# Performance work log

Hardware: AMD Instinct MI355X
Metric: run time of the kernel (lower is better)

The kernel has to match this reference:

```python
import jax, jax.numpy as jnp
import numpy as np

B, S, E = 2, 2048, 1024
H, D = 16, 64
BASE = 10000.0


def rotate_half(x):
    x1, x2 = jnp.split(x, 2, axis=-1)
    return jnp.concatenate((-x2, x1), axis=-1)


def rope_cos_sin(seq_len, dim):
    inv_freq = 1.0 / (BASE ** (jnp.arange(0, dim, 2, dtype=jnp.float32) / dim))
    t = jnp.arange(seq_len, dtype=jnp.float32)
    freqs = jnp.einsum('i,j->ij', t, inv_freq)          # [S, D/2]
    emb = jnp.concatenate((freqs, freqs), axis=-1)       # [S, D]
    return jnp.cos(emb), jnp.sin(emb)


def setup_inputs() -> dict:
    key = jax.random.key(0)
    ks = jax.random.split(key, 9)
    s = 1.0 / np.sqrt(E)
    inp = {
        'x': jax.random.normal(ks[0], (B, S, E), dtype=jnp.float32),
        'mask': jnp.ones((B, S), dtype=jnp.int32),
        'Wq': jax.random.normal(ks[1], (E, H * D), dtype=jnp.float32) * s,
        'bq': jnp.zeros((H * D,), dtype=jnp.float32),
        'Wk': jax.random.normal(ks[2], (E, H * D), dtype=jnp.float32) * s,
        'bk': jnp.zeros((H * D,), dtype=jnp.float32),
        'Wv': jax.random.normal(ks[3], (E, H * D), dtype=jnp.float32) * s,
        'bv': jnp.zeros((H * D,), dtype=jnp.float32),
        'Wo': jax.random.normal(ks[4], (H * D, E), dtype=jnp.float32) * s,
        'bo': jnp.zeros((E,), dtype=jnp.float32),
    }
    return inp


def reference(x, mask, Wq, bq, Wk, bk, Wv, bv, Wo, bo):
    b, s, _ = x.shape
    scale = D ** (-0.5)
    # projections -> [B, H, S, D]
    q = (x @ Wq + bq).reshape(b, s, H, D).transpose(0, 2, 1, 3)
    k = (x @ Wk + bk).reshape(b, s, H, D).transpose(0, 2, 1, 3)
    v = (x @ Wv + bv).reshape(b, s, H, D).transpose(0, 2, 1, 3)
    # rotary position embedding
    cos, sin = rope_cos_sin(s, D)                      # [S, D]
    cos = cos[None, None]
    sin = sin[None, None]
    q = q * cos + rotate_half(q) * sin
    k = k * cos + rotate_half(k) * sin
    # scores [B, H, S, S]
    scores = jnp.einsum('bhqd,bhkd->bhqk', q, k) * scale
    # padding mask [B,1,1,S]
    scores = jnp.where(mask[:, None, None, :] == 0, -jnp.inf, scores)
    # causal mask
    i = jnp.arange(s)
    causal = jnp.where(i[None, :] > i[:, None], -jnp.inf, 0.0)  # [S, S]
    scores = scores + causal[None, None]
    attn = jax.nn.softmax(scores, axis=-1)
    ctx = jnp.einsum('bhqk,bhkd->bhqd', attn, v)
    ctx = ctx.transpose(0, 2, 1, 3).reshape(b, s, H * D)
    return ctx @ Wo + bo
```

## Files before the change

kernel.cpp:

```cpp
#include <hip/hip_runtime.h>
#include <cstdint>
#include <cstddef>

#define DEVI __device__ __forceinline__

typedef __bf16 bf16_t;
typedef __bf16 bf16x4 __attribute__((ext_vector_type(4)));
typedef __bf16 bf16x8 __attribute__((ext_vector_type(8)));
typedef float  f32x4  __attribute__((ext_vector_type(4)));
typedef float  f32x16 __attribute__((ext_vector_type(16)));
typedef unsigned short u16x4 __attribute__((ext_vector_type(4)));
typedef unsigned int   u32x4 __attribute__((ext_vector_type(4)));

static constexpr int Bz = 2, S = 2048, E = 1024, H = 16, Dh = 64;
static constexpr int M  = Bz * S;
static constexpr int N  = H * Dh;
static constexpr int Kd = E;

DEVI unsigned short f2bf(float f) {
  unsigned u = __builtin_bit_cast(unsigned, f);
  return (unsigned short)((u + 0x7fffu + ((u >> 16) & 1u)) >> 16);
}

DEVI void async_copy16(void* lds, const void* g) {
  __builtin_amdgcn_global_load_lds((__attribute__((address_space(1))) void*)(g),
                                   (__attribute__((address_space(3))) void*)(lds), 16, 0, 0);
}

DEVI void block_sync() { asm volatile("s_barrier" ::: "memory"); }
#define VMCNT4() asm volatile("s_waitcnt vmcnt(4)" ::: "memory")
#define VMCNT0() asm volatile("s_waitcnt vmcnt(0)" ::: "memory")

DEVI unsigned cvtpk(float lo, float hi) {
  unsigned r;
  asm("v_cvt_pk_bf16_f32 %0, %1, %2" : "=v"(r) : "v"(lo), "v"(hi));
  return r;
}
DEVI void swap32(unsigned& x, unsigned& y) {
  asm("v_permlane32_swap_b32 %0, %1" : "+v"(x), "+v"(y));
}

__global__ void prep_kernel(const float* __restrict__ x, bf16_t* __restrict__ xb,
                            const float* __restrict__ Wq, const float* __restrict__ Wk,
                            const float* __restrict__ Wv, const float* __restrict__ Wo,
                            bf16_t* __restrict__ WtBase,
                            float* __restrict__ ropeC, float* __restrict__ ropeS) {
  __shared__ unsigned short tile[64][68];
  const int blk = blockIdx.x, tid = threadIdx.x;
  if (blk < 4096) {
    int i = blk * 256 + tid;
    float4 v = ((const float4*)x)[i];
    u16x4 o = { f2bf(v.x), f2bf(v.y), f2bf(v.z), f2bf(v.w) };
    ((u16x4*)xb)[i] = o;
  } else if (blk < 5120) {
    const int i = blk - 4096;
    const int z = i >> 8, rest = i & 255;
    const int n0 = (rest & 15) * 64, k0 = (rest >> 4) * 64;
    const float* W = (z == 0) ? Wq : (z == 1) ? Wk : (z == 2) ? Wv : Wo;
    unsigned short* T = (unsigned short*)(WtBase + (size_t)z * Kd * N);
    for (int e = tid; e < 1024; e += 256) {
      int r = e >> 4, c4 = (e & 15) * 4;
      float4 v = *(const float4*)(W + (size_t)(k0 + r) * N + n0 + c4);
      u16x4 o = { f2bf(v.x), f2bf(v.y), f2bf(v.z), f2bf(v.w) };
      *(u16x4*)&tile[r][c4] = o;
    }
    __syncthreads();
    for (int e = tid; e < 1024; e += 256) {
      int r = e >> 4, c4 = (e & 15) * 4;
      u16x4 o = { tile[c4][r], tile[c4 + 1][r], tile[c4 + 2][r], tile[c4 + 3][r] };
      *(u16x4*)&T[(size_t)(n0 + r) * Kd + k0 + c4] = o;
    }
  } else {
    int i = (blk - 5120) * 256 + tid;
    int pos = i >> 5, j = i & 31;
    float inv = exp2f(-(float)j * 0.41524101186092029f);
    float ang = (float)pos * inv;
    ropeC[i] = cosf(ang);
    ropeS[i] = sinf(ang);
  }
}

__global__ void vtrans_kernel(const bf16_t* __restrict__ V, bf16_t* __restrict__ Vt) {
  __shared__ unsigned short tile[64][68];
  const int bh = blockIdx.y;
  const int s0 = blockIdx.x * 64;
  const unsigned short* Vp = (const unsigned short*)V + (size_t)bh * S * Dh;
  unsigned short* Tp = (unsigned short*)Vt + (size_t)bh * Dh * S;
  const int tid = threadIdx.x;
  for (int e = tid; e < 1024; e += 256) {
    int r = e >> 4, c4 = (e & 15) * 4;
    u16x4 v = *(const u16x4*)(Vp + (size_t)(s0 + r) * Dh + c4);
    *(u16x4*)&tile[r][c4] = v;
  }
  __syncthreads();
  for (int e = tid; e < 1024; e += 256) {
    int d = e >> 4, s4 = (e & 15) * 4;
    u16x4 o = { tile[s4][d], tile[s4 + 1][d], tile[s4 + 2][d], tile[s4 + 3][d] };
    *(u16x4*)&Tp[(size_t)d * S + s0 + s4] = o;
  }
}


DEVI void gemm_mainloop(const bf16_t* __restrict__ A, const bf16_t* __restrict__ Bt,
                        bf16_t* sA, bf16_t* sB, int m0, int n0, f32x4 (&acc)[4][4]) {
  const int tid  = threadIdx.x;
  const int lane = tid & 63;
  const int wid  = tid >> 6;
  const int l16  = lane & 15;
  const int quad = lane >> 4;
  const int wm = (wid >> 1) * 64;
  const int wn = (wid & 1) * 64;
  const int o0 = wid * 2048 + lane * 16;
  const int o1 = o0 + 1024;
  const int r0 = o0 >> 6, c0 = o0 & 63;
  const int r1 = o1 >> 6, c1 = o1 & 63;
  const char* Ab = (const char*)A;
  const char* Bb = (const char*)Bt;
  char* sAc = (char*)sA;
  char* sBc = (char*)sB;

  for (int k0 = 0; k0 < Kd; k0 += 32) {
    __syncthreads();
    async_copy16(sAc + wid * 2048,        Ab + ((size_t)(m0 + r0) * Kd + k0) * 2 + c0);
    async_copy16(sAc + wid * 2048 + 1024, Ab + ((size_t)(m0 + r1) * Kd + k0) * 2 + c1);
    async_copy16(sBc + wid * 2048,        Bb + ((size_t)(n0 + r0) * Kd + k0) * 2 + c0);
    async_copy16(sBc + wid * 2048 + 1024, Bb + ((size_t)(n0 + r1) * Kd + k0) * 2 + c1);
    __syncthreads();
    bf16x8 af[4], bfv[4];
#pragma unroll
    for (int mi = 0; mi < 4; ++mi)
      af[mi] = *(const bf16x8*)(sA + (wm + mi * 16 + l16) * 32 + quad * 8);
#pragma unroll
    for (int ni = 0; ni < 4; ++ni)
      bfv[ni] = *(const bf16x8*)(sB + (wn + ni * 16 + l16) * 32 + quad * 8);
#pragma unroll
    for (int mi = 0; mi < 4; ++mi)
#pragma unroll
      for (int ni = 0; ni < 4; ++ni)
        acc[mi][ni] = __builtin_amdgcn_mfma_f32_16x16x32_bf16(af[mi], bfv[ni], acc[mi][ni], 0, 0, 0);
  }
}

__global__ __launch_bounds__(256, 3) void gemm_qkv_kernel(
    const bf16_t* __restrict__ xb, const bf16_t* __restrict__ WtBase,
    const float* __restrict__ bq, const float* __restrict__ bk, const float* __restrict__ bv,
    bf16_t* __restrict__ outBase,
    const float* __restrict__ ropeC, const float* __restrict__ ropeS) {
  __shared__ bf16_t sA[4096], sB[4096];
  const int z = blockIdx.z;
  const bf16_t* Bt = WtBase + (size_t)z * Kd * N;
  const float* bias = (z == 0) ? bq : (z == 1) ? bk : bv;
  unsigned short* outp = (unsigned short*)(outBase + (size_t)z * M * N);
  const int n0 = blockIdx.x * 128, m0 = blockIdx.y * 128;
  f32x4 acc[4][4] = {};
  gemm_mainloop(xb, Bt, sA, sB, m0, n0, acc);

  const int tid = threadIdx.x, lane = tid & 63, wid = tid >> 6;
  const int l16 = lane & 15, quad = lane >> 4;
  const int wm = (wid >> 1) * 64, wn = (wid & 1) * 64;
  const int cbase = n0 + wn;
  const int h = cbase >> 6;

  if (z < 2) {
    const float qs = (z == 0) ? 0.18033688011112042f : 1.0f;
#pragma unroll
    for (int mi = 0; mi < 4; ++mi)
#pragma unroll
      for (int r = 0; r < 4; ++r) {
        int t = m0 + wm + mi * 16 + quad * 4 + r;
        int bb = t >> 11, s = t & (S - 1);
        size_t obase = ((size_t)(bb * H + h) * S + s) * Dh;
#pragma unroll
        for (int np = 0; np < 2; ++np) {
          int j = np * 16 + l16;
          float cc = ropeC[s * 32 + j];
          float ss = ropeS[s * 32 + j];
          float xlo = acc[mi][np][r]     + bias[cbase + j];
          float xhi = acc[mi][np + 2][r] + bias[cbase + j + 32];
          outp[obase + j]      = f2bf((xlo * cc - xhi * ss) * qs);
          outp[obase + j + 32] = f2bf((xhi * cc + xlo * ss) * qs);
        }
      }
  } else {
#pragma unroll
    for (int mi = 0; mi < 4; ++mi)
#pragma unroll
      for (int r = 0; r < 4; ++r) {
        int t = m0 + wm + mi * 16 + quad * 4 + r;
        int bb = t >> 11, s = t & (S - 1);
        size_t obase = ((size_t)(bb * H + h) * S + s) * Dh;
#pragma unroll
        for (int ni = 0; ni < 4; ++ni) {
          int d = ni * 16 + l16;
          outp[obase + d] = f2bf(acc[mi][ni][r] + bias[cbase + d]);
        }
      }
  }
}

__global__ __launch_bounds__(256, 4) void gemm_o_kernel(
    const bf16_t* __restrict__ A, const bf16_t* __restrict__ Bt,
    const float* __restrict__ bias, float* __restrict__ out) {
  __shared__ bf16_t sA[2048], sB[4096];
  const int n0 = blockIdx.x * 128, m0 = blockIdx.y * 64;
  const int tid = threadIdx.x, lane = tid & 63, wid = tid >> 6;
  const int l16 = lane & 15, quad = lane >> 4;
  const int wm = (wid >> 1) * 32, wn = (wid & 1) * 64;
  const int rowoff = lane >> 2, col8 = (lane & 3) * 8;
  const char* Ab = (const char*)A;
  const char* Bb = (const char*)Bt;
  char* sAc = (char*)sA;
  char* sBc = (char*)sB;
  f32x4 acc[2][4] = {};

  for (int k0 = 0; k0 < Kd; k0 += 32) {
    __syncthreads();
    async_copy16(sAc + wid * 1024,
                 Ab + ((size_t)(m0 + wid * 16 + rowoff) * Kd + k0 + col8) * 2);
    async_copy16(sBc + (wid * 2) * 1024,
                 Bb + ((size_t)(n0 + wid * 32 + rowoff) * Kd + k0 + col8) * 2);
    async_copy16(sBc + (wid * 2 + 1) * 1024,
                 Bb + ((size_t)(n0 + wid * 32 + 16 + rowoff) * Kd + k0 + col8) * 2);
    __syncthreads();
    bf16x8 af[2], bfv[4];
#pragma unroll
    for (int mi = 0; mi < 2; ++mi)
      af[mi] = *(const bf16x8*)(sA + (wm + mi * 16 + l16) * 32 + quad * 8);
#pragma unroll
    for (int ni = 0; ni < 4; ++ni)
      bfv[ni] = *(const bf16x8*)(sB + (wn + ni * 16 + l16) * 32 + quad * 8);
#pragma unroll
    for (int mi = 0; mi < 2; ++mi)
#pragma unroll
      for (int ni = 0; ni < 4; ++ni)
        acc[mi][ni] = __builtin_amdgcn_mfma_f32_16x16x32_bf16(af[mi], bfv[ni], acc[mi][ni], 0, 0, 0);
  }
#pragma unroll
  for (int mi = 0; mi < 2; ++mi)
#pragma unroll
    for (int r = 0; r < 4; ++r) {
      int t = m0 + wm + mi * 16 + quad * 4 + r;
#pragma unroll
      for (int ni = 0; ni < 4; ++ni) {
        int c = n0 + wn + ni * 16 + l16;
        out[(size_t)t * N + c] = acc[mi][ni][r] + bias[c];
      }
    }
}

template <bool MASKED>
DEVI void attn32_phase(const bf16_t* __restrict__ Qp, const char* __restrict__ Kg,
                       const char* __restrict__ Vg, const int* __restrict__ mp,
                       unsigned short* __restrict__ cp, char* lds,
                       int b, int bh, int qb) {
  const int tid = threadIdx.x, lane = tid & 63, wid = tid >> 6;
  const int grp = wid >> 2, w4 = wid & 3;
  const int l32 = lane & 31, hi = lane >> 5;

  const int qw = qb * 128 + w4 * 32;
  const int qg = qw + l32;
  const int nTot = 2 * (qb + 1);
  const int qd = nTot >> 2, rm = nTot & 3;
  const int nG  = qd + ((grp < rm) ? 1 : 0);
  const int st0 = grp * qd + ((grp < rm) ? grp : rm);
  const int nMax = qd + (rm ? 1 : 0);
  const int gk0 = st0 * 64;
  char* gB = lds + grp * 32768;

  bf16x8 qf[4];
#pragma unroll
  for (int c = 0; c < 4; ++c)
    qf[c] = *(const bf16x8*)(Qp + (size_t)(qw + l32) * Dh + c * 16 + hi * 8);
  asm volatile("" :: "v"((float)qf[3][7]));

  int kLds[2], vLds[2], kOff[2], vOff[2];
#pragma unroll
  for (int i = 0; i < 2; ++i) {
    const int s = w4 * 2 + i;
    const int a = s >> 2, c = s & 3;
    kLds[i] = s * 1024;
    kOff[i] = ((a * 32 + l32) * Dh + c * 16 + hi * 8) * 2;
    vLds[i] = 8192 + s * 1024;
    vOff[i] = ((s >> 2) * 32 + l32) * (S * 2) + (((s & 3) * 16 + hi * 8) * 2);
  }

  f32x16 cacc0 = {}, cacc1 = {};
  float lsum = 0.f;

  if (nG > 0) {
    const char* ks = Kg + (size_t)gk0 * (Dh * 2);
    const char* vs = Vg + (size_t)gk0 * 2;
    async_copy16(gB + kLds[0], ks + kOff[0]);
    async_copy16(gB + kLds[1], ks + kOff[1]);
    async_copy16(gB + vLds[0], vs + vOff[0]);
    async_copy16(gB + vLds[1], vs + vOff[1]);
  }

  for (int kt = 0; kt < nMax; ++kt) {
    const int cur = kt & 1;
    const int kb = gk0 + kt * 64;
    const bool act = kt < nG;
    unsigned long long dm = 0;
    if (act) {
      if (kt + 1 < nG) {
        char* dst = gB + (cur ^ 1) * 16384;
        const char* ks = Kg + (size_t)(kb + 64) * (Dh * 2);
        const char* vs = Vg + (size_t)(kb + 64) * 2;
        async_copy16(dst + kLds[0], ks + kOff[0]);
        async_copy16(dst + kLds[1], ks + kOff[1]);
        async_copy16(dst + vLds[0], vs + vOff[0]);
        async_copy16(dst + vLds[1], vs + vOff[1]);
        if (!MASKED) { VMCNT4(); }
      } else if (!MASKED) {
        VMCNT0();
      }
      if (MASKED) {
        int mk = mp[kb + lane];
        VMCNT0();
        dm = __ballot(mk == 0);
      }
    }
    block_sync();

    if (act) {
      const bf16_t* sK = (const bf16_t*)(gB + cur * 16384);
      const bf16_t* sV = (const bf16_t*)(gB + cur * 16384 + 8192);
      const bool needC = (kb + 63 > qw);

#pragma unroll
      for (int a = 0; a < 2; ++a) {
        f32x16 st = {};
        __builtin_amdgcn_s_setprio(1);
#pragma unroll
        for (int c = 0; c < 4; ++c) {
          bf16x8 kf = *(const bf16x8*)(sK + (a * 4 + c) * 512 + lane * 8);
          st = __builtin_amdgcn_mfma_f32_32x32x16_bf16(kf, qf[c], st, 0, 0, 0);
        }
        __builtin_amdgcn_s_setprio(0);
        if (MASKED && dm) {
#pragma unroll
          for (int r = 0; r < 16; ++r)
            if ((dm >> (a * 32 + (r & 3) + 8 * (r >> 2) + 4 * hi)) & 1ull) st[r] = -1e30f;
        }
        if (needC) {
          const int kbase = kb + a * 32 + 4 * hi - qg;
#pragma unroll
          for (int r = 0; r < 16; ++r)
            if (kbase + (r & 3) + 8 * (r >> 2) > 0) st[r] = -1e30f;
        }
        unsigned P0[4], P1[4];
#pragma unroll
        for (int m = 0; m < 4; ++m) {
          float p0 = exp2f(st[4 * m + 0]), p1 = exp2f(st[4 * m + 1]);
          float p2 = exp2f(st[4 * m + 2]), p3 = exp2f(st[4 * m + 3]);
          lsum += (p0 + p1) + (p2 + p3);
          P0[m] = cvtpk(p0, p1);
          P1[m] = cvtpk(p2, p3);
        }
        swap32(P0[0], P0[1]); swap32(P1[0], P1[1]);
        swap32(P0[2], P0[3]); swap32(P1[2], P1[3]);
        u32x4 t0 = { P0[0], P1[0], P0[1], P1[1] };
        u32x4 t1 = { P0[2], P1[2], P0[3], P1[3] };
        const bf16x8 f0 = __builtin_bit_cast(bf16x8, t0);
        const bf16x8 f1 = __builtin_bit_cast(bf16x8, t1);
        __builtin_amdgcn_s_setprio(1);
        {
          bf16x8 v00 = *(const bf16x8*)(sV + (0 + a * 2 + 0) * 512 + lane * 8);
          cacc0 = __builtin_amdgcn_mfma_f32_32x32x16_bf16(v00, f0, cacc0, 0, 0, 0);
          bf16x8 v01 = *(const bf16x8*)(sV + (0 + a * 2 + 1) * 512 + lane * 8);
          cacc0 = __builtin_amdgcn_mfma_f32_32x32x16_bf16(v01, f1, cacc0, 0, 0, 0);
          bf16x8 v10 = *(const bf16x8*)(sV + (4 + a * 2 + 0) * 512 + lane * 8);
          cacc1 = __builtin_amdgcn_mfma_f32_32x32x16_bf16(v10, f0, cacc1, 0, 0, 0);
          bf16x8 v11 = *(const bf16x8*)(sV + (4 + a * 2 + 1) * 512 + lane * 8);
          cacc1 = __builtin_amdgcn_mfma_f32_32x32x16_bf16(v11, f1, cacc1, 0, 0, 0);
        }
        __builtin_amdgcn_s_setprio(0);
      }
    }
    block_sync();
  }

  if (grp != 0) {
    char* rb = lds + (size_t)((grp - 1) * 4 + w4) * 8448;
#pragma unroll
    for (int c = 0; c < 4; ++c) {
      f32x4 v = { cacc0[4 * c], cacc0[4 * c + 1], cacc0[4 * c + 2], cacc0[4 * c + 3] };
      *(f32x4*)(rb + c * 1024 + lane * 16) = v;
    }
#pragma unroll
    for (int c = 0; c < 4; ++c) {
      f32x4 v = { cacc1[4 * c], cacc1[4 * c + 1], cacc1[4 * c + 2], cacc1[4 * c + 3] };
      *(f32x4*)(rb + (4 + c) * 1024 + lane * 16) = v;
    }
    *(float*)(rb + 8192 + lane * 4) = lsum;
  }
  asm volatile("s_waitcnt lgkmcnt(0)" ::: "memory");
  block_sync();
  if (grp == 0) {
#pragma unroll
    for (int j = 1; j < 4; ++j) {
      const char* rb = lds + (size_t)((j - 1) * 4 + w4) * 8448;
#pragma unroll
      for (int c = 0; c < 4; ++c) {
        f32x4 v = *(const f32x4*)(rb + c * 1024 + lane * 16);
        cacc0[4 * c] += v[0]; cacc0[4 * c + 1] += v[1];
        cacc0[4 * c + 2] += v[2]; cacc0[4 * c + 3] += v[3];
      }
#pragma unroll
      for (int c = 0; c < 4; ++c) {
        f32x4 v = *(const f32x4*)(rb + (4 + c) * 1024 + lane * 16);
        cacc1[4 * c] += v[0]; cacc1[4 * c + 1] += v[1];
        cacc1[4 * c + 2] += v[2]; cacc1[4 * c + 3] += v[3];
      }
      lsum += *(const float*)(rb + 8192 + lane * 4);
    }
    lsum += __shfl_xor(lsum, 32);
    const float inv = 1.0f / lsum;
    const size_t base = ((size_t)(b * S + qw + l32)) * N + (size_t)(bh & 15) * Dh;
#pragma unroll
    for (int m = 0; m < 4; ++m) {
      const int d0 = m * 8 + 4 * hi;
      u16x4 o0 = { f2bf(cacc0[4 * m + 0] * inv), f2bf(cacc0[4 * m + 1] * inv),
                   f2bf(cacc0[4 * m + 2] * inv), f2bf(cacc0[4 * m + 3] * inv) };
      *(u16x4*)&cp[base + d0] = o0;
      u16x4 o1 = { f2bf(cacc1[4 * m + 0] * inv), f2bf(cacc1[4 * m + 1] * inv),
                   f2bf(cacc1[4 * m + 2] * inv), f2bf(cacc1[4 * m + 3] * inv) };
      *(u16x4*)&cp[base + 32 + d0] = o1;
    }
  }
  block_sync();
}

__global__ __launch_bounds__(1024, 4) void attn_kernel(
    const bf16_t* __restrict__ Q, const bf16_t* __restrict__ Kb,
    const bf16_t* __restrict__ Vt, const int* __restrict__ mask,
    bf16_t* __restrict__ ctx) {
  __shared__ f32x4 ldsbuf[8192];

  const int idx = blockIdx.x;
  const int p   = idx >> 5;
  const int bh  = idx & 31;
  const int qbL = 15 - p, qbS = p;
  const int b   = bh >> 4;
  const int lane = threadIdx.x & 63;

  const bf16_t* Qp = Q + (size_t)bh * S * Dh;
  const char*   Kg = (const char*)(Kb + (size_t)bh * S * Dh);
  const char*   Vg = (const char*)(Vt + (size_t)bh * Dh * S);
  const int*    mp = mask + b * S;

  int dead = 0;
  const int4* mp4 = (const int4*)mp;
  for (int c = lane; c < S / 4; c += 64) {
    int4 m = mp4[c];
    dead |= (m.x == 0) | (m.y == 0) | (m.z == 0) | (m.w == 0);
  }
  const bool anydead = __ballot(dead != 0) != 0ull;

  unsigned short* cp = (unsigned short*)ctx;
  char* lds = (char*)ldsbuf;
  if (!anydead) {
#pragma unroll 1
    for (int t = 0; t < 2; ++t)
      attn32_phase<false>(Qp, Kg, Vg, mp, cp, lds, b, bh, t ? qbS : qbL);
  } else {
#pragma unroll 1
    for (int t = 0; t < 2; ++t)
      attn32_phase<true>(Qp, Kg, Vg, mp, cp, lds, b, bh, t ? qbS : qbL);
  }
}


extern "C" void kernel_launch(void* const* d_in, const int* in_sizes, int n_in,
                              void* d_out, int out_size, void* d_ws, size_t ws_size,
                              hipStream_t stream) {
  const float* x  = (const float*)d_in[0];
  const int*  msk = (const int*)d_in[1];
  const float* Wq = (const float*)d_in[2];
  const float* bq = (const float*)d_in[3];
  const float* Wk = (const float*)d_in[4];
  const float* bk = (const float*)d_in[5];
  const float* Wv = (const float*)d_in[6];
  const float* bv = (const float*)d_in[7];
  const float* Wo = (const float*)d_in[8];
  const float* bo = (const float*)d_in[9];
  float* out = (float*)d_out;
  (void)in_sizes; (void)n_in; (void)out_size; (void)ws_size;

  char* ws = (char*)d_ws;
  bf16_t* xb   = (bf16_t*)(ws);
  bf16_t* WT   = (bf16_t*)(ws + (8u  << 20));
  bf16_t* qkv  = (bf16_t*)(ws + (16u << 20));
  bf16_t* Qb   = qkv;
  bf16_t* Kbuf = qkv + (size_t)1 * M * N;
  bf16_t* Vb   = qkv + (size_t)2 * M * N;
  bf16_t* Vt   = xb;
  bf16_t* ctx  = Vb;
  float* ropeC = (float*)(ws + (40u << 20));
  float* ropeS = ropeC + (size_t)S * 32;

  prep_kernel<<<5376, 256, 0, stream>>>(x, xb, Wq, Wk, Wv, Wo, WT, ropeC, ropeS);
  gemm_qkv_kernel<<<dim3(8, 32, 3), 256, 0, stream>>>(xb, WT, bq, bk, bv, qkv, ropeC, ropeS);
  vtrans_kernel<<<dim3(32, 32), 256, 0, stream>>>(Vb, Vt);
  attn_kernel<<<256, 1024, 0, stream>>>(Qb, Kbuf, Vt, msk, ctx);
  gemm_o_kernel<<<dim3(8, 64), 256, 0, stream>>>(ctx, WT + (size_t)3 * Kd * N, bo, out);
}
```

Measured before the change: 224.2 us.

## Split attention into 64-query tiles with 512-thread blocks and swizzled LDS reduction

Attention now runs 512 blocks of 512 threads. Each block handles 64-query tiles instead of 128-query tiles, with four key-split groups of two waves, and each group steps through 32-key chunks. One wave of each pair loads K and the other loads V. The cross-group reduction now lands in a swizzled LDS layout, and all waves share the final sum and bf16 store instead of only group 0. This is meant to raise the block count and spread the causal work more evenly across CUs, with a cheaper reduction, at the cost of more barriers per key chunk and smaller MFMA batches per sync.

```diff
diff --git a/kernel.cpp b/kernel.cpp
--- a/kernel.cpp
+++ b/kernel.cpp
@@ -252,20 +252,20 @@
 DEVI void attn32_phase(const bf16_t* __restrict__ Qp, const char* __restrict__ Kg,
                        const char* __restrict__ Vg, const int* __restrict__ mp,
                        unsigned short* __restrict__ cp, char* lds,
-                       int b, int bh, int qb) {
+                       int b, int bh, int qt) {
   const int tid = threadIdx.x, lane = tid & 63, wid = tid >> 6;
-  const int grp = wid >> 2, w4 = wid & 3;
+  const int grp = wid >> 1, w2 = wid & 1;
   const int l32 = lane & 31, hi = lane >> 5;
 
-  const int qw = qb * 128 + w4 * 32;
+  const int qw = qt * 64 + w2 * 32;
   const int qg = qw + l32;
-  const int nTot = 2 * (qb + 1);
-  const int qd = nTot >> 2, rm = nTot & 3;
+  const int nk = 2 * (qt + 1);
+  const int qd = nk >> 2, rm = nk & 3;
   const int nG  = qd + ((grp < rm) ? 1 : 0);
   const int st0 = grp * qd + ((grp < rm) ? grp : rm);
   const int nMax = qd + (rm ? 1 : 0);
-  const int gk0 = st0 * 64;
-  char* gB = lds + grp * 32768;
+  const int gk0 = st0 * 32;
+  char* gB = lds + grp * 16384;
 
   bf16x8 qf[4];
 #pragma unroll
@@ -273,49 +273,45 @@
     qf[c] = *(const bf16x8*)(Qp + (size_t)(qw + l32) * Dh + c * 16 + hi * 8);
   asm volatile("" :: "v"((float)qf[3][7]));
 
-  int kLds[2], vLds[2], kOff[2], vOff[2];
-#pragma unroll
-  for (int i = 0; i < 2; ++i) {
-    const int s = w4 * 2 + i;
-    const int a = s >> 2, c = s & 3;
-    kLds[i] = s * 1024;
-    kOff[i] = ((a * 32 + l32) * Dh + c * 16 + hi * 8) * 2;
-    vLds[i] = 8192 + s * 1024;
-    vOff[i] = ((s >> 2) * 32 + l32) * (S * 2) + (((s & 3) * 16 + hi * 8) * 2);
+  const char* gsrc = w2 ? Vg : Kg;
+  const size_t keyB = w2 ? 2u : 128u;
+  int sLds[4], sOff[4];
+#pragma unroll
+  for (int i = 0; i < 4; ++i) {
+    sLds[i] = (w2 * 4 + i) * 1024;
+    if (w2 == 0) sOff[i] = (l32 * 64 + i * 16 + hi * 8) * 2;
+    else {
+      int e = i >> 1, kc = i & 1;
+      sOff[i] = ((e * 32 + l32) * S + kc * 16 + hi * 8) * 2;
+    }
   }
 
   f32x16 cacc0 = {}, cacc1 = {};
   float lsum = 0.f;
 
   if (nG > 0) {
-    const char* ks = Kg + (size_t)gk0 * (Dh * 2);
-    const char* vs = Vg + (size_t)gk0 * 2;
-    async_copy16(gB + kLds[0], ks + kOff[0]);
-    async_copy16(gB + kLds[1], ks + kOff[1]);
-    async_copy16(gB + vLds[0], vs + vOff[0]);
-    async_copy16(gB + vLds[1], vs + vOff[1]);
+    const char* bp = gsrc + (size_t)gk0 * keyB;
+#pragma unroll
+    for (int i = 0; i < 4; ++i) async_copy16(gB + sLds[i], bp + sOff[i]);
   }
 
   for (int kt = 0; kt < nMax; ++kt) {
     const int cur = kt & 1;
-    const int kb = gk0 + kt * 64;
+    const int kb = gk0 + kt * 32;
     const bool act = kt < nG;
     unsigned long long dm = 0;
     if (act) {
       if (kt + 1 < nG) {
-        char* dst = gB + (cur ^ 1) * 16384;
-        const char* ks = Kg + (size_t)(kb + 64) * (Dh * 2);
-        const char* vs = Vg + (size_t)(kb + 64) * 2;
-        async_copy16(dst + kLds[0], ks + kOff[0]);
-        async_copy16(dst + kLds[1], ks + kOff[1]);
-        async_copy16(dst + vLds[0], vs + vOff[0]);
-        async_copy16(dst + vLds[1], vs + vOff[1]);
+        const char* bp = gsrc + (size_t)(kb + 32) * keyB;
+        char* dst = gB + (cur ^ 1) * 8192;
+#pragma unroll
+        for (int i = 0; i < 4; ++i) async_copy16(dst + sLds[i], bp + sOff[i]);
         if (!MASKED) { VMCNT4(); }
       } else if (!MASKED) {
         VMCNT0();
       }
       if (MASKED) {
-        int mk = mp[kb + lane];
+        int mk = mp[kb + l32];
         VMCNT0();
         dm = __ballot(mk == 0);
       }
@@ -323,124 +319,108 @@
     block_sync();
 
     if (act) {
-      const bf16_t* sK = (const bf16_t*)(gB + cur * 16384);
-      const bf16_t* sV = (const bf16_t*)(gB + cur * 16384 + 8192);
-      const bool needC = (kb + 63 > qw);
-
-#pragma unroll
-      for (int a = 0; a < 2; ++a) {
-        f32x16 st = {};
-        __builtin_amdgcn_s_setprio(1);
-#pragma unroll
-        for (int c = 0; c < 4; ++c) {
-          bf16x8 kf = *(const bf16x8*)(sK + (a * 4 + c) * 512 + lane * 8);
-          st = __builtin_amdgcn_mfma_f32_32x32x16_bf16(kf, qf[c], st, 0, 0, 0);
-        }
-        __builtin_amdgcn_s_setprio(0);
-        if (MASKED && dm) {
-#pragma unroll
-          for (int r = 0; r < 16; ++r)
-            if ((dm >> (a * 32 + (r & 3) + 8 * (r >> 2) + 4 * hi)) & 1ull) st[r] = -1e30f;
-        }
-        if (needC) {
-          const int kbase = kb + a * 32 + 4 * hi - qg;
-#pragma unroll
-          for (int r = 0; r < 16; ++r)
-            if (kbase + (r & 3) + 8 * (r >> 2) > 0) st[r] = -1e30f;
-        }
-        unsigned P0[4], P1[4];
-#pragma unroll
-        for (int m = 0; m < 4; ++m) {
-          float p0 = exp2f(st[4 * m + 0]), p1 = exp2f(st[4 * m + 1]);
-          float p2 = exp2f(st[4 * m + 2]), p3 = exp2f(st[4 * m + 3]);
-          lsum += (p0 + p1) + (p2 + p3);
-          P0[m] = cvtpk(p0, p1);
-          P1[m] = cvtpk(p2, p3);
-        }
-        swap32(P0[0], P0[1]); swap32(P1[0], P1[1]);
-        swap32(P0[2], P0[3]); swap32(P1[2], P1[3]);
-        u32x4 t0 = { P0[0], P1[0], P0[1], P1[1] };
-        u32x4 t1 = { P0[2], P1[2], P0[3], P1[3] };
-        const bf16x8 f0 = __builtin_bit_cast(bf16x8, t0);
-        const bf16x8 f1 = __builtin_bit_cast(bf16x8, t1);
-        __builtin_amdgcn_s_setprio(1);
-        {
-          bf16x8 v00 = *(const bf16x8*)(sV + (0 + a * 2 + 0) * 512 + lane * 8);
-          cacc0 = __builtin_amdgcn_mfma_f32_32x32x16_bf16(v00, f0, cacc0, 0, 0, 0);
-          bf16x8 v01 = *(const bf16x8*)(sV + (0 + a * 2 + 1) * 512 + lane * 8);
-          cacc0 = __builtin_amdgcn_mfma_f32_32x32x16_bf16(v01, f1, cacc0, 0, 0, 0);
-          bf16x8 v10 = *(const bf16x8*)(sV + (4 + a * 2 + 0) * 512 + lane * 8);
-          cacc1 = __builtin_amdgcn_mfma_f32_32x32x16_bf16(v10, f0, cacc1, 0, 0, 0);
-          bf16x8 v11 = *(const bf16x8*)(sV + (4 + a * 2 + 1) * 512 + lane * 8);
-          cacc1 = __builtin_amdgcn_mfma_f32_32x32x16_bf16(v11, f1, cacc1, 0, 0, 0);
-        }
-        __builtin_amdgcn_s_setprio(0);
-      }
+      const bf16_t* sT = (const bf16_t*)(gB + cur * 8192);
+      f32x16 st = {};
+      __builtin_amdgcn_s_setprio(1);
+#pragma unroll
+      for (int c = 0; c < 4; ++c) {
+        bf16x8 kf = *(const bf16x8*)(sT + c * 512 + lane * 8);
+        st = __builtin_amdgcn_mfma_f32_32x32x16_bf16(kf, qf[c], st, 0, 0, 0);
+      }
+      __builtin_amdgcn_s_setprio(0);
+      if (MASKED && dm) {
+#pragma unroll
+        for (int r = 0; r < 16; ++r)
+          if ((dm >> ((r & 3) + 8 * (r >> 2) + 4 * hi)) & 1ull) st[r] = -1e30f;
+      }
+      if (kb + 31 > qw) {
+        const int kbase = kb + 4 * hi - qg;
+#pragma unroll
+        for (int r = 0; r < 16; ++r)
+          if (kbase + (r & 3) + 8 * (r >> 2) > 0) st[r] = -1e30f;
+      }
+      unsigned P0[4], P1[4];
+#pragma unroll
+      for (int m = 0; m < 4; ++m) {
+        float p0 = exp2f(st[4 * m + 0]), p1 = exp2f(st[4 * m + 1]);
+        float p2 = exp2f(st[4 * m + 2]), p3 = exp2f(st[4 * m + 3]);
+        lsum += (p0 + p1) + (p2 + p3);
+        P0[m] = cvtpk(p0, p1);
+        P1[m] = cvtpk(p2, p3);
+      }
+      swap32(P0[0], P0[1]); swap32(P1[0], P1[1]);
+      swap32(P0[2], P0[3]); swap32(P1[2], P1[3]);
+      u32x4 t0 = { P0[0], P1[0], P0[1], P1[1] };
+      u32x4 t1 = { P0[2], P1[2], P0[3], P1[3] };
+      const bf16x8 f0 = __builtin_bit_cast(bf16x8, t0);
+      const bf16x8 f1 = __builtin_bit_cast(bf16x8, t1);
+      __builtin_amdgcn_s_setprio(1);
+      {
+        bf16x8 v00 = *(const bf16x8*)(sT + 2048 + 0 * 512 + lane * 8);
+        cacc0 = __builtin_amdgcn_mfma_f32_32x32x16_bf16(v00, f0, cacc0, 0, 0, 0);
+        bf16x8 v01 = *(const bf16x8*)(sT + 2048 + 1 * 512 + lane * 8);
+        cacc0 = __builtin_amdgcn_mfma_f32_32x32x16_bf16(v01, f1, cacc0, 0, 0, 0);
+        bf16x8 v10 = *(const bf16x8*)(sT + 2048 + 2 * 512 + lane * 8);
+        cacc1 = __builtin_amdgcn_mfma_f32_32x32x16_bf16(v10, f0, cacc1, 0, 0, 0);
+        bf16x8 v11 = *(const bf16x8*)(sT + 2048 + 3 * 512 + lane * 8);
+        cacc1 = __builtin_amdgcn_mfma_f32_32x32x16_bf16(v11, f1, cacc1, 0, 0, 0);
+      }
+      __builtin_amdgcn_s_setprio(0);
     }
     block_sync();
   }
 
-  if (grp != 0) {
-    char* rb = lds + (size_t)((grp - 1) * 4 + w4) * 8448;
-#pragma unroll
-    for (int c = 0; c < 4; ++c) {
-      f32x4 v = { cacc0[4 * c], cacc0[4 * c + 1], cacc0[4 * c + 2], cacc0[4 * c + 3] };
-      *(f32x4*)(rb + c * 1024 + lane * 16) = v;
-    }
-#pragma unroll
-    for (int c = 0; c < 4; ++c) {
-      f32x4 v = { cacc1[4 * c], cacc1[4 * c + 1], cacc1[4 * c + 2], cacc1[4 * c + 3] };
-      *(f32x4*)(rb + (4 + c) * 1024 + lane * 16) = v;
-    }
-    *(float*)(rb + 8192 + lane * 4) = lsum;
+  float* reg = (float*)lds;
+  {
+    const int row = w2 * 32 + l32;
+    float* rb = reg + grp * 4096 + row * 64;
+#pragma unroll
+    for (int m = 0; m < 4; ++m) {
+      f32x4 v = { cacc0[4 * m], cacc0[4 * m + 1], cacc0[4 * m + 2], cacc0[4 * m + 3] };
+      *(f32x4*)(rb + ((8 * m + 4 * hi + 4 * row) & 63)) = v;
+    }
+#pragma unroll
+    for (int m = 0; m < 4; ++m) {
+      f32x4 v = { cacc1[4 * m], cacc1[4 * m + 1], cacc1[4 * m + 2], cacc1[4 * m + 3] };
+      *(f32x4*)(rb + ((32 + 8 * m + 4 * hi + 4 * row) & 63)) = v;
+    }
+    reg[16384 + (grp * 2 + hi) * 64 + row] = lsum;
   }
   asm volatile("s_waitcnt lgkmcnt(0)" ::: "memory");
   block_sync();
-  if (grp == 0) {
-#pragma unroll
-    for (int j = 1; j < 4; ++j) {
-      const char* rb = lds + (size_t)((j - 1) * 4 + w4) * 8448;
-#pragma unroll
-      for (int c = 0; c < 4; ++c) {
-        f32x4 v = *(const f32x4*)(rb + c * 1024 + lane * 16);
-        cacc0[4 * c] += v[0]; cacc0[4 * c + 1] += v[1];
-        cacc0[4 * c + 2] += v[2]; cacc0[4 * c + 3] += v[3];
-      }
-#pragma unroll
-      for (int c = 0; c < 4; ++c) {
-        f32x4 v = *(const f32x4*)(rb + (4 + c) * 1024 + lane * 16);
-        cacc1[4 * c] += v[0]; cacc1[4 * c + 1] += v[1];
-        cacc1[4 * c + 2] += v[2]; cacc1[4 * c + 3] += v[3];
-      }
-      lsum += *(const float*)(rb + 8192 + lane * 4);
-    }
-    lsum += __shfl_xor(lsum, 32);
-    const float inv = 1.0f / lsum;
-    const size_t base = ((size_t)(b * S + qw + l32)) * N + (size_t)(bh & 15) * Dh;
-#pragma unroll
-    for (int m = 0; m < 4; ++m) {
-      const int d0 = m * 8 + 4 * hi;
-      u16x4 o0 = { f2bf(cacc0[4 * m + 0] * inv), f2bf(cacc0[4 * m + 1] * inv),
-                   f2bf(cacc0[4 * m + 2] * inv), f2bf(cacc0[4 * m + 3] * inv) };
-      *(u16x4*)&cp[base + d0] = o0;
-      u16x4 o1 = { f2bf(cacc1[4 * m + 0] * inv), f2bf(cacc1[4 * m + 1] * inv),
-                   f2bf(cacc1[4 * m + 2] * inv), f2bf(cacc1[4 * m + 3] * inv) };
-      *(u16x4*)&cp[base + 32 + d0] = o1;
-    }
+  {
+    const int orow = wid * 8 + (lane & 7);
+    const int d0 = (lane >> 3) * 8;
+    f32x4 oa = {}, ob = {};
+    float ls = 0.f;
+#pragma unroll
+    for (int g = 0; g < 4; ++g) {
+      const float* rb = reg + g * 4096 + orow * 64;
+      f32x4 va = *(const f32x4*)(rb + ((d0 + 4 * orow) & 63));
+      f32x4 vb = *(const f32x4*)(rb + ((d0 + 4 + 4 * orow) & 63));
+      oa += va; ob += vb;
+      ls += reg[16384 + (g * 2 + 0) * 64 + orow] + reg[16384 + (g * 2 + 1) * 64 + orow];
+    }
+    const float inv = 1.0f / ls;
+    const size_t base = ((size_t)(b * S + qt * 64 + orow)) * N + (size_t)(bh & 15) * Dh + d0;
+    u16x4 o0 = { f2bf(oa[0] * inv), f2bf(oa[1] * inv), f2bf(oa[2] * inv), f2bf(oa[3] * inv) };
+    u16x4 o1 = { f2bf(ob[0] * inv), f2bf(ob[1] * inv), f2bf(ob[2] * inv), f2bf(ob[3] * inv) };
+    *(u16x4*)&cp[base] = o0;
+    *(u16x4*)&cp[base + 4] = o1;
   }
   block_sync();
 }
 
-__global__ __launch_bounds__(1024, 4) void attn_kernel(
+__global__ __launch_bounds__(512, 4) void attn_kernel(
     const bf16_t* __restrict__ Q, const bf16_t* __restrict__ Kb,
     const bf16_t* __restrict__ Vt, const int* __restrict__ mask,
     bf16_t* __restrict__ ctx) {
-  __shared__ f32x4 ldsbuf[8192];
+  __shared__ f32x4 ldsbuf[4224];
 
   const int idx = blockIdx.x;
   const int p   = idx >> 5;
   const int bh  = idx & 31;
-  const int qbL = 15 - p, qbS = p;
+  const int qtL = 31 - p, qtS = p;
   const int b   = bh >> 4;
   const int lane = threadIdx.x & 63;
 
@@ -460,13 +440,11 @@
   unsigned short* cp = (unsigned short*)ctx;
   char* lds = (char*)ldsbuf;
   if (!anydead) {
-#pragma unroll 1
-    for (int t = 0; t < 2; ++t)
-      attn32_phase<false>(Qp, Kg, Vg, mp, cp, lds, b, bh, t ? qbS : qbL);
+    attn32_phase<false>(Qp, Kg, Vg, mp, cp, lds, b, bh, qtL);
+    attn32_phase<false>(Qp, Kg, Vg, mp, cp, lds, b, bh, qtS);
   } else {
-#pragma unroll 1
-    for (int t = 0; t < 2; ++t)
-      attn32_phase<true>(Qp, Kg, Vg, mp, cp, lds, b, bh, t ? qbS : qbL);
+    attn32_phase<true>(Qp, Kg, Vg, mp, cp, lds, b, bh, qtL);
+    attn32_phase<true>(Qp, Kg, Vg, mp, cp, lds, b, bh, qtS);
   }
 }
 
@@ -502,6 +480,6 @@
   prep_kernel<<<5376, 256, 0, stream>>>(x, xb, Wq, Wk, Wv, Wo, WT, ropeC, ropeS);
   gemm_qkv_kernel<<<dim3(8, 32, 3), 256, 0, stream>>>(xb, WT, bq, bk, bv, qkv, ropeC, ropeS);
   vtrans_kernel<<<dim3(32, 32), 256, 0, stream>>>(Vb, Vt);
-  attn_kernel<<<256, 1024, 0, stream>>>(Qb, Kbuf, Vt, msk, ctx);
+  attn_kernel<<<512, 512, 0, stream>>>(Qb, Kbuf, Vt, msk, ctx);
   gemm_o_kernel<<<dim3(8, 64), 256, 0, stream>>>(ctx, WT + (size_t)3 * Kd * N, bo, out);
 }
```

New measurement: 201.8 us. 1.11x faster.
